# Kernel optimization log

Measured on AMD Instinct MI355X. Metric: run time of the kernel, lower is better.

## Reference

```python
import jax, jax.numpy as jnp
import numpy as np

N_NODES = 100000
N_EDGES = 640000
H_FEATS = 128


def setup_inputs() -> dict:
    key = jax.random.key(0)
    k_h, k_src, k_dst, k_w1, k_b1, k_w2, k_b2 = jax.random.split(key, 7)
    h = jax.random.normal(k_h, (N_NODES, H_FEATS), dtype=jnp.float32)
    src = jax.random.randint(k_src, (N_EDGES,), 0, N_NODES, dtype=jnp.int64)
    dst = jax.random.randint(k_dst, (N_EDGES,), 0, N_NODES, dtype=jnp.int64)
    # nn.Linear params: W1 (h_feats, 2*h_feats) as (out, in); store transposed for x @ W
    lim1 = 1.0 / np.sqrt(2 * H_FEATS)
    W1 = jax.random.uniform(k_w1, (2 * H_FEATS, H_FEATS), jnp.float32, -lim1, lim1)
    b1 = jax.random.uniform(k_b1, (H_FEATS,), jnp.float32, -lim1, lim1)
    lim2 = 1.0 / np.sqrt(H_FEATS)
    W2 = jax.random.uniform(k_w2, (H_FEATS, 1), jnp.float32, -lim2, lim2)
    b2 = jax.random.uniform(k_b2, (1,), jnp.float32, -lim2, lim2)
    return {"h": h, "src": src, "dst": dst, "W1": W1, "b1": b1, "W2": W2, "b2": b2}


def reference(h, src, dst, W1, b1, W2, b2):
    # gather src/dst node features per edge and concat: [E, 2*h_feats]
    he = jnp.concatenate([h[src], h[dst]], axis=1)
    hidden = jax.nn.relu(he @ W1 + b1)          # [E, h_feats]
    score = (hidden @ W2 + b2)[:, 0]            # [E]
    return score
```

## Files before the change

### kernel.cpp

```cpp
#include <hip/hip_runtime.h>

#define N_NODES 100000
#define N_EDGES 640000
#define F 128
#define NT 6250
#define NBLK 512

typedef __attribute__((ext_vector_type(8))) short short8;
typedef __attribute__((ext_vector_type(4))) float float4v;

static __device__ __forceinline__ unsigned short f2bf(float f) {
    unsigned int u = __float_as_uint(f);
    u += 0x7fffu + ((u >> 16) & 1u);
    return (unsigned short)(u >> 16);
}

__global__ __launch_bounds__(256) void prep_wt(
    const float* __restrict__ W1, unsigned short* __restrict__ Wt)
{
    int id = blockIdx.x * 256 + threadIdx.x;
    int n = id >> 7, k = id & 127;
    float v = W1[((n & 128) + k) * 128 + (n & 127)];
    Wt[id] = f2bf(v);
}

__global__ __launch_bounds__(256, 2) void node_proj(
    const float* __restrict__ h, const unsigned short* __restrict__ Wt,
    const float* __restrict__ b1,
    unsigned short* __restrict__ A, unsigned short* __restrict__ B)
{
    __shared__ unsigned short w_swz[256 * 128];
    __shared__ unsigned short hb[16 * 136];
    __shared__ unsigned short oA[16 * 136];
    __shared__ unsigned short oB[16 * 136];

    const int tid  = threadIdx.x;
    const int lane = tid & 63;
    const int l16  = lane & 15;
    const int quad = lane >> 4;
    const int w    = tid >> 6;

#pragma unroll
    for (int i = 0; i < 16; ++i) {
        int cl = i * 256 + tid;
        int r = cl >> 4, c = cl & 15;
        uint4 v = *(const uint4*)(Wt + (size_t)r * F + c * 8);
        *(uint4*)&w_swz[((r << 4) + (c ^ (r & 15))) * 8] = v;
    }

    const bool isA = (w < 2);
    const int colb = (w & 1) * 64;
    float4 bv[4];
#pragma unroll
    for (int p = 0; p < 4; ++p) {
        int col = colb + p * 16 + quad * 4;
        bv[p] = isA ? *(const float4*)(b1 + col) : make_float4(0.f, 0.f, 0.f, 0.f);
    }
    unsigned short* ostage = isA ? oA : oB;

    int srow[2], sc4[2];
#pragma unroll
    for (int i = 0; i < 2; ++i) { int f = i * 256 + tid; srow[i] = f >> 5; sc4[i] = f & 31; }

#define LOADH(PF, T)                                                           \
    _Pragma("unroll") for (int i = 0; i < 2; ++i)                              \
        PF[i] = *(const float4*)(h + ((size_t)(T) * 16 + srow[i]) * F + sc4[i] * 4);

#define CVTWRITE(PF)                                                           \
    _Pragma("unroll") for (int i = 0; i < 2; ++i) {                            \
        uint2 p;                                                               \
        p.x = (unsigned)f2bf(PF[i].x) | ((unsigned)f2bf(PF[i].y) << 16);       \
        p.y = (unsigned)f2bf(PF[i].z) | ((unsigned)f2bf(PF[i].w) << 16);       \
        *(uint2*)&hb[srow[i] * 136 + sc4[i] * 4] = p;                          \
    }

    int t = blockIdx.x;
    float4 pf[2];
    LOADH(pf, t); CVTWRITE(pf);
    __syncthreads();

    while (t < NT) {
        const int tn = t + NBLK;
        const bool actn = (tn < NT);
        if (actn) LOADH(pf, tn);

        float4v acc[4];
#pragma unroll
        for (int p = 0; p < 4; ++p) acc[p] = (float4v){0.f, 0.f, 0.f, 0.f};
#pragma unroll
        for (int k0 = 0; k0 < 4; ++k0) {
            short8 bf = *(const short8*)&hb[l16 * 136 + k0 * 32 + quad * 8];
            const int cc = (k0 * 4 + quad);
#pragma unroll
            for (int p = 0; p < 4; ++p) {
                const int row = w * 64 + p * 16 + l16;
                short8 af = *(const short8*)&w_swz[((row << 4) + (cc ^ l16)) * 8];
                acc[p] = __builtin_amdgcn_mfma_f32_16x16x32_bf16(af, bf, acc[p], 0, 0, 0);
            }
        }
        __syncthreads();

        if (actn) CVTWRITE(pf);
#pragma unroll
        for (int p = 0; p < 4; ++p) {
            ushort4 sv;
            sv.x = f2bf(acc[p][0] + bv[p].x);
            sv.y = f2bf(acc[p][1] + bv[p].y);
            sv.z = f2bf(acc[p][2] + bv[p].z);
            sv.w = f2bf(acc[p][3] + bv[p].w);
            *(ushort4*)&ostage[l16 * 136 + colb + p * 16 + quad * 4] = sv;
        }
        __syncthreads();

        {
            const int r = tid >> 4, c = tid & 15;
            const size_t goff = ((size_t)t * 16 + r) * F + c * 8;
            *(uint4*)(A + goff) = *(const uint4*)&oA[r * 136 + c * 8];
            *(uint4*)(B + goff) = *(const uint4*)&oB[r * 136 + c * 8];
        }
        t = tn;
    }
#undef LOADH
#undef CVTWRITE
}

__global__ __launch_bounds__(256) void edge_score(
    const unsigned short* __restrict__ A, const unsigned short* __restrict__ B,
    const int* __restrict__ src, const int* __restrict__ dst,
    const float* __restrict__ W2, const float* __restrict__ b2,
    float* __restrict__ out)
{
    const int tid = threadIdx.x;
    const int sub = tid & 7;
    const int e0  = blockIdx.x * 128 + (tid >> 3) * 4;

    const int4 sv = *(const int4*)(src + e0);
    const int4 dv = *(const int4*)(dst + e0);
    const int s[4] = {sv.x, sv.y, sv.z, sv.w};
    const int d[4] = {dv.x, dv.y, dv.z, dv.w};

    uint4 av0[4], av1[4], bv0[4], bv1[4];
#pragma unroll
    for (int i = 0; i < 4; ++i) {
        const unsigned short* Ar = A + (size_t)s[i] * F;
        const unsigned short* Br = B + (size_t)d[i] * F;
        av0[i] = *(const uint4*)(Ar + sub * 8);
        av1[i] = *(const uint4*)(Ar + 64 + sub * 8);
        bv0[i] = *(const uint4*)(Br + sub * 8);
        bv1[i] = *(const uint4*)(Br + 64 + sub * 8);
    }

    const float4 w0 = *(const float4*)(W2 + sub * 8);
    const float4 w1 = *(const float4*)(W2 + sub * 8 + 4);
    const float4 w2 = *(const float4*)(W2 + 64 + sub * 8);
    const float4 w3 = *(const float4*)(W2 + 64 + sub * 8 + 4);
    const float bias = b2[0];

#define TERM(UA, UB, WL, WH)                                                   \
    {                                                                          \
        float fa0 = __uint_as_float((UA) << 16);                               \
        float fa1 = __uint_as_float((UA) & 0xFFFF0000u);                       \
        float fb0 = __uint_as_float((UB) << 16);                               \
        float fb1 = __uint_as_float((UB) & 0xFFFF0000u);                       \
        sacc = fmaf(fmaxf(fa0 + fb0, 0.f), (WL), sacc);                        \
        sacc = fmaf(fmaxf(fa1 + fb1, 0.f), (WH), sacc);                        \
    }
#pragma unroll
    for (int i = 0; i < 4; ++i) {
        float sacc = 0.f;
        TERM(av0[i].x, bv0[i].x, w0.x, w0.y)
        TERM(av0[i].y, bv0[i].y, w0.z, w0.w)
        TERM(av0[i].z, bv0[i].z, w1.x, w1.y)
        TERM(av0[i].w, bv0[i].w, w1.z, w1.w)
        TERM(av1[i].x, bv1[i].x, w2.x, w2.y)
        TERM(av1[i].y, bv1[i].y, w2.z, w2.w)
        TERM(av1[i].z, bv1[i].z, w3.x, w3.y)
        TERM(av1[i].w, bv1[i].w, w3.z, w3.w)
        sacc += __shfl_xor(sacc, 1);
        sacc += __shfl_xor(sacc, 2);
        sacc += __shfl_xor(sacc, 4);
        if (sub == 0) out[e0 + i] = sacc + bias;
    }
#undef TERM
}

extern "C" void kernel_launch(void* const* d_in, const int* in_sizes, int n_in,
                              void* d_out, int out_size, void* d_ws, size_t ws_size,
                              hipStream_t stream) {
    const float* h   = (const float*)d_in[0];
    const int*   src = (const int*)d_in[1];
    const int*   dst = (const int*)d_in[2];
    const float* W1  = (const float*)d_in[3];
    const float* b1  = (const float*)d_in[4];
    const float* W2  = (const float*)d_in[5];
    const float* b2  = (const float*)d_in[6];
    float* out = (float*)d_out;

    unsigned short* Wt = (unsigned short*)d_ws;
    unsigned short* A  = Wt + 256 * 128;
    unsigned short* B  = A + (size_t)N_NODES * F;

    prep_wt<<<128, 256, 0, stream>>>(W1, Wt);
    node_proj<<<NBLK, 256, 0, stream>>>(h, Wt, b1, A, B);
    edge_score<<<N_EDGES / 128, 256, 0, stream>>>(A, B, src, dst, W2, b2, out);
}
```

Before: 156.5 us.

## Fuse weight prep, node projection and edge scoring into one cooperative kernel

Merges the three kernels into a single cooperative launch with grid-wide syncs between the weight transpose, node projection and edge scoring phases. The edge phase becomes a grid-stride loop over 512 blocks instead of 5000 independent blocks. The intent is to remove two kernel launch gaps. In exchange it pays for grid.sync costs, and the gather phase now runs at the lower occupancy imposed by the projection's 64KB+ shared memory and launch bounds, which may hurt latency hiding in the random gathers.

After: 320.9 us. 2.05x slower.

```diff
diff --git a/kernel.cpp b/kernel.cpp
--- a/kernel.cpp
+++ b/kernel.cpp
@@ -1,4 +1,7 @@
 #include <hip/hip_runtime.h>
+#include <hip/hip_cooperative_groups.h>
+
+namespace cg = cooperative_groups;
 
 #define N_NODES 100000
 #define N_EDGES 640000
@@ -15,52 +18,56 @@
     return (unsigned short)(u >> 16);
 }
 
-__global__ __launch_bounds__(256) void prep_wt(
-    const float* __restrict__ W1, unsigned short* __restrict__ Wt)
-{
-    int id = blockIdx.x * 256 + threadIdx.x;
-    int n = id >> 7, k = id & 127;
-    float v = W1[((n & 128) + k) * 128 + (n & 127)];
-    Wt[id] = f2bf(v);
-}
-
-__global__ __launch_bounds__(256, 2) void node_proj(
-    const float* __restrict__ h, const unsigned short* __restrict__ Wt,
-    const float* __restrict__ b1,
-    unsigned short* __restrict__ A, unsigned short* __restrict__ B)
+__global__ __launch_bounds__(256, 2) void fused_gnn(
+    const float* __restrict__ h, const int* __restrict__ src,
+    const int* __restrict__ dst, const float* __restrict__ W1,
+    const float* __restrict__ b1, const float* __restrict__ W2,
+    const float* __restrict__ b2, unsigned short* __restrict__ Wt,
+    unsigned short* __restrict__ A, unsigned short* __restrict__ B,
+    float* __restrict__ out)
 {
     __shared__ unsigned short w_swz[256 * 128];
     __shared__ unsigned short hb[16 * 136];
     __shared__ unsigned short oA[16 * 136];
     __shared__ unsigned short oB[16 * 136];
 
-    const int tid  = threadIdx.x;
-    const int lane = tid & 63;
-    const int l16  = lane & 15;
-    const int quad = lane >> 4;
-    const int w    = tid >> 6;
-
-#pragma unroll
-    for (int i = 0; i < 16; ++i) {
-        int cl = i * 256 + tid;
-        int r = cl >> 4, c = cl & 15;
-        uint4 v = *(const uint4*)(Wt + (size_t)r * F + c * 8);
-        *(uint4*)&w_swz[((r << 4) + (c ^ (r & 15))) * 8] = v;
-    }
-
-    const bool isA = (w < 2);
-    const int colb = (w & 1) * 64;
-    float4 bv[4];
-#pragma unroll
-    for (int p = 0; p < 4; ++p) {
-        int col = colb + p * 16 + quad * 4;
-        bv[p] = isA ? *(const float4*)(b1 + col) : make_float4(0.f, 0.f, 0.f, 0.f);
-    }
-    unsigned short* ostage = isA ? oA : oB;
-
-    int srow[2], sc4[2];
-#pragma unroll
-    for (int i = 0; i < 2; ++i) { int f = i * 256 + tid; srow[i] = f >> 5; sc4[i] = f & 31; }
+    const int tid = threadIdx.x;
+    cg::grid_group grid = cg::this_grid();
+
+    if (blockIdx.x < 128) {
+        int id = blockIdx.x * 256 + tid;
+        int n = id >> 7, k = id & 127;
+        Wt[id] = f2bf(W1[((n & 128) + k) * 128 + (n & 127)]);
+    }
+    grid.sync();
+
+    {
+        const int lane = tid & 63;
+        const int l16  = lane & 15;
+        const int quad = lane >> 4;
+        const int w    = tid >> 6;
+
+#pragma unroll
+        for (int i = 0; i < 16; ++i) {
+            int cl = i * 256 + tid;
+            int r = cl >> 4, c = cl & 15;
+            uint4 v = *(const uint4*)(Wt + (size_t)r * F + c * 8);
+            *(uint4*)&w_swz[((r << 4) + (c ^ (r & 15))) * 8] = v;
+        }
+
+        const bool isA = (w < 2);
+        const int colb = (w & 1) * 64;
+        float4 bv[4];
+#pragma unroll
+        for (int p = 0; p < 4; ++p) {
+            int col = colb + p * 16 + quad * 4;
+            bv[p] = isA ? *(const float4*)(b1 + col) : make_float4(0.f, 0.f, 0.f, 0.f);
+        }
+        unsigned short* ostage = isA ? oA : oB;
+
+        int srow[2], sc4[2];
+#pragma unroll
+        for (int i = 0; i < 2; ++i) { int f = i * 256 + tid; srow[i] = f >> 5; sc4[i] = f & 31; }
 
 #define LOADH(PF, T)                                                           \
     _Pragma("unroll") for (int i = 0; i < 2; ++i)                              \
@@ -74,87 +81,85 @@
         *(uint2*)&hb[srow[i] * 136 + sc4[i] * 4] = p;                          \
     }
 
-    int t = blockIdx.x;
-    float4 pf[2];
-    LOADH(pf, t); CVTWRITE(pf);
-    __syncthreads();
-
-    while (t < NT) {
-        const int tn = t + NBLK;
-        const bool actn = (tn < NT);
-        if (actn) LOADH(pf, tn);
-
-        float4v acc[4];
-#pragma unroll
-        for (int p = 0; p < 4; ++p) acc[p] = (float4v){0.f, 0.f, 0.f, 0.f};
-#pragma unroll
-        for (int k0 = 0; k0 < 4; ++k0) {
-            short8 bf = *(const short8*)&hb[l16 * 136 + k0 * 32 + quad * 8];
-            const int cc = (k0 * 4 + quad);
+        int t = blockIdx.x;
+        float4 pf[2];
+        LOADH(pf, t); CVTWRITE(pf);
+        __syncthreads();
+
+        while (t < NT) {
+            const int tn = t + NBLK;
+            const bool actn = (tn < NT);
+            if (actn) LOADH(pf, tn);
+
+            float4v acc[4];
+#pragma unroll
+            for (int p = 0; p < 4; ++p) acc[p] = (float4v){0.f, 0.f, 0.f, 0.f};
+#pragma unroll
+            for (int k0 = 0; k0 < 4; ++k0) {
+                short8 bf = *(const short8*)&hb[l16 * 136 + k0 * 32 + quad * 8];
+                const int cc = (k0 * 4 + quad);
+#pragma unroll
+                for (int p = 0; p < 4; ++p) {
+                    const int row = w * 64 + p * 16 + l16;
+                    short8 af = *(const short8*)&w_swz[((row << 4) + (cc ^ l16)) * 8];
+                    acc[p] = __builtin_amdgcn_mfma_f32_16x16x32_bf16(af, bf, acc[p], 0, 0, 0);
+                }
+            }
+            __syncthreads();
+
+            if (actn) CVTWRITE(pf);
 #pragma unroll
             for (int p = 0; p < 4; ++p) {
-                const int row = w * 64 + p * 16 + l16;
-                short8 af = *(const short8*)&w_swz[((row << 4) + (cc ^ l16)) * 8];
-                acc[p] = __builtin_amdgcn_mfma_f32_16x16x32_bf16(af, bf, acc[p], 0, 0, 0);
-            }
-        }
-        __syncthreads();
-
-        if (actn) CVTWRITE(pf);
-#pragma unroll
-        for (int p = 0; p < 4; ++p) {
-            ushort4 sv;
-            sv.x = f2bf(acc[p][0] + bv[p].x);
-            sv.y = f2bf(acc[p][1] + bv[p].y);
-            sv.z = f2bf(acc[p][2] + bv[p].z);
-            sv.w = f2bf(acc[p][3] + bv[p].w);
-            *(ushort4*)&ostage[l16 * 136 + colb + p * 16 + quad * 4] = sv;
-        }
-        __syncthreads();
-
-        {
-            const int r = tid >> 4, c = tid & 15;
-            const size_t goff = ((size_t)t * 16 + r) * F + c * 8;
-            *(uint4*)(A + goff) = *(const uint4*)&oA[r * 136 + c * 8];
-            *(uint4*)(B + goff) = *(const uint4*)&oB[r * 136 + c * 8];
-        }
-        t = tn;
-    }
+                ushort4 sv;
+                sv.x = f2bf(acc[p][0] + bv[p].x);
+                sv.y = f2bf(acc[p][1] + bv[p].y);
+                sv.z = f2bf(acc[p][2] + bv[p].z);
+                sv.w = f2bf(acc[p][3] + bv[p].w);
+                *(ushort4*)&ostage[l16 * 136 + colb + p * 16 + quad * 4] = sv;
+            }
+            __syncthreads();
+
+            {
+                const int r = tid >> 4, c = tid & 15;
+                const size_t goff = ((size_t)t * 16 + r) * F + c * 8;
+                *(uint4*)(A + goff) = *(const uint4*)&oA[r * 136 + c * 8];
+                *(uint4*)(B + goff) = *(const uint4*)&oB[r * 136 + c * 8];
+            }
+            t = tn;
+        }
 #undef LOADH
 #undef CVTWRITE
-}
-
-__global__ __launch_bounds__(256) void edge_score(
-    const unsigned short* __restrict__ A, const unsigned short* __restrict__ B,
-    const int* __restrict__ src, const int* __restrict__ dst,
-    const float* __restrict__ W2, const float* __restrict__ b2,
-    float* __restrict__ out)
-{
-    const int tid = threadIdx.x;
-    const int sub = tid & 7;
-    const int e0  = blockIdx.x * 128 + (tid >> 3) * 4;
-
-    const int4 sv = *(const int4*)(src + e0);
-    const int4 dv = *(const int4*)(dst + e0);
-    const int s[4] = {sv.x, sv.y, sv.z, sv.w};
-    const int d[4] = {dv.x, dv.y, dv.z, dv.w};
-
-    uint4 av0[4], av1[4], bv0[4], bv1[4];
-#pragma unroll
-    for (int i = 0; i < 4; ++i) {
-        const unsigned short* Ar = A + (size_t)s[i] * F;
-        const unsigned short* Br = B + (size_t)d[i] * F;
-        av0[i] = *(const uint4*)(Ar + sub * 8);
-        av1[i] = *(const uint4*)(Ar + 64 + sub * 8);
-        bv0[i] = *(const uint4*)(Br + sub * 8);
-        bv1[i] = *(const uint4*)(Br + 64 + sub * 8);
-    }
-
-    const float4 w0 = *(const float4*)(W2 + sub * 8);
-    const float4 w1 = *(const float4*)(W2 + sub * 8 + 4);
-    const float4 w2 = *(const float4*)(W2 + 64 + sub * 8);
-    const float4 w3 = *(const float4*)(W2 + 64 + sub * 8 + 4);
-    const float bias = b2[0];
+    }
+
+    __threadfence();
+    grid.sync();
+
+    {
+        const int sub = tid & 7;
+        const float4 w0 = *(const float4*)(W2 + sub * 8);
+        const float4 w1 = *(const float4*)(W2 + sub * 8 + 4);
+        const float4 w2 = *(const float4*)(W2 + 64 + sub * 8);
+        const float4 w3 = *(const float4*)(W2 + 64 + sub * 8 + 4);
+        const float bias = b2[0];
+
+        for (int eb = blockIdx.x; eb < N_EDGES / 128; eb += NBLK) {
+            const int e0 = eb * 128 + (tid >> 3) * 4;
+
+            const int4 sv = *(const int4*)(src + e0);
+            const int4 dv = *(const int4*)(dst + e0);
+            const int s[4] = {sv.x, sv.y, sv.z, sv.w};
+            const int d[4] = {dv.x, dv.y, dv.z, dv.w};
+
+            uint4 av0[4], av1[4], bv0[4], bv1[4];
+#pragma unroll
+            for (int i = 0; i < 4; ++i) {
+                const unsigned short* Ar = A + (size_t)s[i] * F;
+                const unsigned short* Br = B + (size_t)d[i] * F;
+                av0[i] = *(const uint4*)(Ar + sub * 8);
+                av1[i] = *(const uint4*)(Ar + 64 + sub * 8);
+                bv0[i] = *(const uint4*)(Br + sub * 8);
+                bv1[i] = *(const uint4*)(Br + 64 + sub * 8);
+            }
 
 #define TERM(UA, UB, WL, WH)                                                   \
     {                                                                          \
@@ -166,22 +171,24 @@
         sacc = fmaf(fmaxf(fa1 + fb1, 0.f), (WH), sacc);                        \
     }
 #pragma unroll
-    for (int i = 0; i < 4; ++i) {
-        float sacc = 0.f;
-        TERM(av0[i].x, bv0[i].x, w0.x, w0.y)
-        TERM(av0[i].y, bv0[i].y, w0.z, w0.w)
-        TERM(av0[i].z, bv0[i].z, w1.x, w1.y)
-        TERM(av0[i].w, bv0[i].w, w1.z, w1.w)
-        TERM(av1[i].x, bv1[i].x, w2.x, w2.y)
-        TERM(av1[i].y, bv1[i].y, w2.z, w2.w)
-        TERM(av1[i].z, bv1[i].z, w3.x, w3.y)
-        TERM(av1[i].w, bv1[i].w, w3.z, w3.w)
-        sacc += __shfl_xor(sacc, 1);
-        sacc += __shfl_xor(sacc, 2);
-        sacc += __shfl_xor(sacc, 4);
-        if (sub == 0) out[e0 + i] = sacc + bias;
-    }
+            for (int i = 0; i < 4; ++i) {
+                float sacc = 0.f;
+                TERM(av0[i].x, bv0[i].x, w0.x, w0.y)
+                TERM(av0[i].y, bv0[i].y, w0.z, w0.w)
+                TERM(av0[i].z, bv0[i].z, w1.x, w1.y)
+                TERM(av0[i].w, bv0[i].w, w1.z, w1.w)
+                TERM(av1[i].x, bv1[i].x, w2.x, w2.y)
+                TERM(av1[i].y, bv1[i].y, w2.z, w2.w)
+                TERM(av1[i].z, bv1[i].z, w3.x, w3.y)
+                TERM(av1[i].w, bv1[i].w, w3.z, w3.w)
+                sacc += __shfl_xor(sacc, 1);
+                sacc += __shfl_xor(sacc, 2);
+                sacc += __shfl_xor(sacc, 4);
+                if (sub == 0) out[e0 + i] = sacc + bias;
+            }
 #undef TERM
+        }
+    }
 }
 
 extern "C" void kernel_launch(void* const* d_in, const int* in_sizes, int n_in,
@@ -200,7 +207,9 @@
     unsigned short* A  = Wt + 256 * 128;
     unsigned short* B  = A + (size_t)N_NODES * F;
 
-    prep_wt<<<128, 256, 0, stream>>>(W1, Wt);
-    node_proj<<<NBLK, 256, 0, stream>>>(h, Wt, b1, A, B);
-    edge_score<<<N_EDGES / 128, 256, 0, stream>>>(A, B, src, dst, W2, b2, out);
+    void* args[] = {(void*)&h, (void*)&src, (void*)&dst, (void*)&W1, (void*)&b1,
+                    (void*)&W2, (void*)&b2, (void*)&Wt, (void*)&A, (void*)&B,
+                    (void*)&out};
+    hipLaunchCooperativeKernel((const void*)fused_gnn, dim3(NBLK), dim3(256),
+                               args, 0, stream);
 }
```
